# Optimization experiments

Hardware: AMD Instinct MI355X
Metric: run time of the kernel (lower is better)

The kernel has to match this reference:

```python
import jax, jax.numpy as jnp
import numpy as np

EPS = 1e-8  # numerical guard in padded (masked) softmax denominator


def setup_inputs() -> dict:
    key = jax.random.key(0)
    k1, k2 = jax.random.split(key)
    B, N, D = 8, 2048, 3
    coordinates = jax.random.normal(k1, (B, N, D), dtype=jnp.float32)
    masks = (jax.random.uniform(k2, (B, N, N)) < 0.9).astype(jnp.float32)
    sigma = jnp.ones((1,), dtype=jnp.float32)  # NonNeg learned scalar
    return {"coordinates": coordinates, "masks": masks, "sigma": sigma}


def reference(coordinates, masks, sigma):
    # pairwise squared euclidean distances: ||xi||^2 - 2 xi.xj + ||xj||^2
    norms = jnp.sum(coordinates ** 2, axis=-1, keepdims=True)            # [B,N,1]
    inner = jnp.einsum('bnd,bmd->bnm', coordinates, coordinates)         # [B,N,N]
    distances = norms - 2.0 * inner + jnp.swapaxes(norms, -1, -2)        # [B,N,N]
    # Gaussian kernel
    A = jnp.exp(-distances / (sigma ** 2))                               # [B,N,N]
    # padded_softmax: mask then row-normalize (A is positive, so this is a
    # masked softmax over -d/sigma^2 along the last axis)
    A = A * masks
    return A / (jnp.sum(A, axis=-1, keepdims=True) + EPS)
```

## Files before the change

kernel.cpp:

```cpp
#include <hip/hip_runtime.h>
#include <math.h>


#define NN      2048
#define THREADS 512
#define ROWS_PER_BLOCK 16
#define EPS     1e-8f

typedef float vf4 __attribute__((ext_vector_type(4)));

__global__ __launch_bounds__(THREADS, 8) void gauss_adj_kernel(
    const float* __restrict__ coords,
    const float* __restrict__ masks,
    const float* __restrict__ sigma,
    float* __restrict__ out)
{
    const int tid  = threadIdx.x;
    const int wid  = tid >> 6;
    const int lane = tid & 63;
    const int base = blockIdx.x * ROWS_PER_BLOCK;
    const int b    = base >> 11;

    __shared__ __align__(16) float qx[NN];
    __shared__ __align__(16) float qy[NN];
    __shared__ __align__(16) float qz[NN];
    __shared__ __align__(16) float qw[NN];

    const float s = sigma[0];
    const float C = 1.44269504088896341f / (s * s);
    const float twoC = 2.0f * C;
    const float* cb = coords + (size_t)b * NN * 3;

    for (int idx = tid; idx < NN; idx += THREADS) {
        const float x = cb[idx * 3 + 0];
        const float y = cb[idx * 3 + 1];
        const float z = cb[idx * 3 + 2];
        qx[idx] = twoC * x;
        qy[idx] = twoC * y;
        qz[idx] = twoC * z;
        qw[idx] = -C * (x * x + y * y + z * z);
    }
    __syncthreads();

    const vf4* qx4 = (const vf4*)qx;
    const vf4* qy4 = (const vf4*)qy;
    const vf4* qz4 = (const vf4*)qz;
    const vf4* qw4 = (const vf4*)qw;

    #pragma unroll
    for (int g = 0; g < 2; ++g) {
        const int row = base + (g << 3) + wid;
        const int i   = row & (NN - 1);

        const float xi = cb[i * 3 + 0];
        const float yi = cb[i * 3 + 1];
        const float zi = cb[i * 3 + 2];

        const vf4* mrow = (const vf4*)(masks + (size_t)row * NN);
        vf4*       orow = (vf4*)(out + (size_t)row * NN);

        vf4 a[8];
        #pragma unroll
        for (int w = 0; w < 8; ++w) a[w] = mrow[w * 64 + lane];

        float lsum = 0.0f;
        #pragma unroll
        for (int w = 0; w < 8; ++w) {
            const int q_ = w * 64 + lane;
            const vf4 X = qx4[q_], Y = qy4[q_], Z = qz4[q_], W = qw4[q_];
            vf4 v = a[w];
            v.x *= exp2f(fmaf(xi, X.x, fmaf(yi, Y.x, fmaf(zi, Z.x, W.x))));
            v.y *= exp2f(fmaf(xi, X.y, fmaf(yi, Y.y, fmaf(zi, Z.y, W.y))));
            v.z *= exp2f(fmaf(xi, X.z, fmaf(yi, Y.z, fmaf(zi, Z.z, W.z))));
            v.w *= exp2f(fmaf(xi, X.w, fmaf(yi, Y.w, fmaf(zi, Z.w, W.w))));
            a[w] = v;
            lsum += (v.x + v.y) + (v.z + v.w);
        }

        #pragma unroll
        for (int off = 32; off > 0; off >>= 1)
            lsum += __shfl_xor(lsum, off, 64);
        const float inv = 1.0f / (lsum + EPS);

        #pragma unroll
        for (int w = 0; w < 8; ++w) {
            vf4 o = a[w];
            o.x *= inv; o.y *= inv; o.z *= inv; o.w *= inv;
            __builtin_nontemporal_store(o, &orow[w * 64 + lane]);
        }
    }
}

extern "C" void kernel_launch(void* const* d_in, const int* in_sizes, int n_in,
                              void* d_out, int out_size, void* d_ws, size_t ws_size,
                              hipStream_t stream) {
    const float* coords = (const float*)d_in[0];
    const float* masks  = (const float*)d_in[1];
    const float* sigma  = (const float*)d_in[2];
    float* out = (float*)d_out;

    const int B    = in_sizes[0] / (NN * 3);
    const int rows = B * NN;
    gauss_adj_kernel<<<rows / ROWS_PER_BLOCK, THREADS, 0, stream>>>(coords, masks, sigma, out);
}
```

Baseline: 274.3 us.

## Split fused kernel into row-sum pass and recompute-normalize pass

```diff
diff --git a/kernel.cpp b/kernel.cpp
--- a/kernel.cpp
+++ b/kernel.cpp
@@ -4,33 +4,16 @@
 
 #define NN      2048
 #define THREADS 512
-#define ROWS_PER_BLOCK 16
+#define RPB     8
 #define EPS     1e-8f
 
 typedef float vf4 __attribute__((ext_vector_type(4)));
 
-__global__ __launch_bounds__(THREADS, 8) void gauss_adj_kernel(
-    const float* __restrict__ coords,
-    const float* __restrict__ masks,
-    const float* __restrict__ sigma,
-    float* __restrict__ out)
+__device__ __forceinline__ void stage_q(const float* __restrict__ cb,
+                                        float C, float twoC,
+                                        float* qx, float* qy, float* qz, float* qw,
+                                        int tid)
 {
-    const int tid  = threadIdx.x;
-    const int wid  = tid >> 6;
-    const int lane = tid & 63;
-    const int base = blockIdx.x * ROWS_PER_BLOCK;
-    const int b    = base >> 11;
-
-    __shared__ __align__(16) float qx[NN];
-    __shared__ __align__(16) float qy[NN];
-    __shared__ __align__(16) float qz[NN];
-    __shared__ __align__(16) float qw[NN];
-
-    const float s = sigma[0];
-    const float C = 1.44269504088896341f / (s * s);
-    const float twoC = 2.0f * C;
-    const float* cb = coords + (size_t)b * NN * 3;
-
     for (int idx = tid; idx < NN; idx += THREADS) {
         const float x = cb[idx * 3 + 0];
         const float y = cb[idx * 3 + 1];
@@ -40,54 +23,104 @@
         qz[idx] = twoC * z;
         qw[idx] = -C * (x * x + y * y + z * z);
     }
+}
+
+__global__ __launch_bounds__(THREADS, 8) void gauss_sum_kernel(
+    const float* __restrict__ coords,
+    const float* __restrict__ masks,
+    const float* __restrict__ sigma,
+    float* __restrict__ sums)
+{
+    const int tid  = threadIdx.x;
+    const int wid  = tid >> 6;
+    const int lane = tid & 63;
+    const int base = blockIdx.x * RPB;
+    const int b    = base >> 11;
+
+    __shared__ __align__(16) float qx[NN], qy[NN], qz[NN], qw[NN];
+
+    const float s = sigma[0];
+    const float C = 1.44269504088896341f / (s * s);
+    const float* cb = coords + (size_t)b * NN * 3;
+    stage_q(cb, C, 2.0f * C, qx, qy, qz, qw, tid);
     __syncthreads();
 
+    const int row = base + wid;
+    const int i   = row & (NN - 1);
+    const float xi = cb[i * 3 + 0];
+    const float yi = cb[i * 3 + 1];
+    const float zi = cb[i * 3 + 2];
+
+    const vf4* mrow = (const vf4*)(masks + (size_t)row * NN);
+    const vf4* qx4 = (const vf4*)qx;
+    const vf4* qy4 = (const vf4*)qy;
+    const vf4* qz4 = (const vf4*)qz;
+    const vf4* qw4 = (const vf4*)qw;
+
+    float lsum = 0.0f;
+    #pragma unroll
+    for (int w = 0; w < 8; ++w) {
+        const int q_ = w * 64 + lane;
+        const vf4 m = mrow[q_];
+        const vf4 X = qx4[q_], Y = qy4[q_], Z = qz4[q_], W = qw4[q_];
+        lsum += m.x * exp2f(fmaf(xi, X.x, fmaf(yi, Y.x, fmaf(zi, Z.x, W.x))));
+        lsum += m.y * exp2f(fmaf(xi, X.y, fmaf(yi, Y.y, fmaf(zi, Z.y, W.y))));
+        lsum += m.z * exp2f(fmaf(xi, X.z, fmaf(yi, Y.z, fmaf(zi, Z.z, W.z))));
+        lsum += m.w * exp2f(fmaf(xi, X.w, fmaf(yi, Y.w, fmaf(zi, Z.w, W.w))));
+    }
+
+    #pragma unroll
+    for (int off = 32; off > 0; off >>= 1)
+        lsum += __shfl_xor(lsum, off, 64);
+    if (lane == 0) sums[row] = lsum;
+}
+
+__global__ __launch_bounds__(THREADS, 8) void gauss_norm_kernel(
+    const float* __restrict__ coords,
+    const float* __restrict__ masks,
+    const float* __restrict__ sigma,
+    const float* __restrict__ sums,
+    float* __restrict__ out)
+{
+    const int tid  = threadIdx.x;
+    const int wid  = tid >> 6;
+    const int lane = tid & 63;
+    const int base = blockIdx.x * RPB;
+    const int b    = base >> 11;
+
+    __shared__ __align__(16) float qx[NN], qy[NN], qz[NN], qw[NN];
+
+    const float s = sigma[0];
+    const float C = 1.44269504088896341f / (s * s);
+    const float* cb = coords + (size_t)b * NN * 3;
+    stage_q(cb, C, 2.0f * C, qx, qy, qz, qw, tid);
+    __syncthreads();
+
+    const int row = base + wid;
+    const int i   = row & (NN - 1);
+    const float xi = cb[i * 3 + 0];
+    const float yi = cb[i * 3 + 1];
+    const float zi = cb[i * 3 + 2];
+    const float inv = 1.0f / (sums[row] + EPS);
+
+    const vf4* mrow = (const vf4*)(masks + (size_t)row * NN);
+    vf4*       orow = (vf4*)(out + (size_t)row * NN);
     const vf4* qx4 = (const vf4*)qx;
     const vf4* qy4 = (const vf4*)qy;
     const vf4* qz4 = (const vf4*)qz;
     const vf4* qw4 = (const vf4*)qw;
 
     #pragma unroll
-    for (int g = 0; g < 2; ++g) {
-        const int row = base + (g << 3) + wid;
-        const int i   = row & (NN - 1);
-
-        const float xi = cb[i * 3 + 0];
-        const float yi = cb[i * 3 + 1];
-        const float zi = cb[i * 3 + 2];
-
-        const vf4* mrow = (const vf4*)(masks + (size_t)row * NN);
-        vf4*       orow = (vf4*)(out + (size_t)row * NN);
-
-        vf4 a[8];
-        #pragma unroll
-        for (int w = 0; w < 8; ++w) a[w] = mrow[w * 64 + lane];
-
-        float lsum = 0.0f;
-        #pragma unroll
-        for (int w = 0; w < 8; ++w) {
-            const int q_ = w * 64 + lane;
-            const vf4 X = qx4[q_], Y = qy4[q_], Z = qz4[q_], W = qw4[q_];
-            vf4 v = a[w];
-            v.x *= exp2f(fmaf(xi, X.x, fmaf(yi, Y.x, fmaf(zi, Z.x, W.x))));
-            v.y *= exp2f(fmaf(xi, X.y, fmaf(yi, Y.y, fmaf(zi, Z.y, W.y))));
-            v.z *= exp2f(fmaf(xi, X.z, fmaf(yi, Y.z, fmaf(zi, Z.z, W.z))));
-            v.w *= exp2f(fmaf(xi, X.w, fmaf(yi, Y.w, fmaf(zi, Z.w, W.w))));
-            a[w] = v;
-            lsum += (v.x + v.y) + (v.z + v.w);
-        }
-
-        #pragma unroll
-        for (int off = 32; off > 0; off >>= 1)
-            lsum += __shfl_xor(lsum, off, 64);
-        const float inv = 1.0f / (lsum + EPS);
-
-        #pragma unroll
-        for (int w = 0; w < 8; ++w) {
-            vf4 o = a[w];
-            o.x *= inv; o.y *= inv; o.z *= inv; o.w *= inv;
-            __builtin_nontemporal_store(o, &orow[w * 64 + lane]);
-        }
+    for (int w = 0; w < 8; ++w) {
+        const int q_ = w * 64 + lane;
+        const vf4 m = mrow[q_];
+        const vf4 X = qx4[q_], Y = qy4[q_], Z = qz4[q_], W = qw4[q_];
+        vf4 o;
+        o.x = m.x * exp2f(fmaf(xi, X.x, fmaf(yi, Y.x, fmaf(zi, Z.x, W.x)))) * inv;
+        o.y = m.y * exp2f(fmaf(xi, X.y, fmaf(yi, Y.y, fmaf(zi, Z.y, W.y)))) * inv;
+        o.z = m.z * exp2f(fmaf(xi, X.z, fmaf(yi, Y.z, fmaf(zi, Z.z, W.z)))) * inv;
+        o.w = m.w * exp2f(fmaf(xi, X.w, fmaf(yi, Y.w, fmaf(zi, Z.w, W.w)))) * inv;
+        __builtin_nontemporal_store(o, &orow[q_]);
     }
 }
 
@@ -97,9 +130,12 @@
     const float* coords = (const float*)d_in[0];
     const float* masks  = (const float*)d_in[1];
     const float* sigma  = (const float*)d_in[2];
-    float* out = (float*)d_out;
+    float* out  = (float*)d_out;
+    float* sums = (float*)d_ws;
 
     const int B    = in_sizes[0] / (NN * 3);
     const int rows = B * NN;
-    gauss_adj_kernel<<<rows / ROWS_PER_BLOCK, THREADS, 0, stream>>>(coords, masks, sigma, out);
+    const int grid = rows / RPB;
+    gauss_sum_kernel<<<grid, THREADS, 0, stream>>>(coords, masks, sigma, sums);
+    gauss_norm_kernel<<<grid, THREADS, 0, stream>>>(coords, masks, sigma, sums, out);
 }
```

After: 257.7 us. 6.1% less time.
